# Performance work log

Measured on AMD Instinct MI355X. Metric: run time of the kernel, lower is better.

## Reference

```python
import jax, jax.numpy as jnp
import numpy as np

B, T, C, H = 4, 2048, 1024, 16
HD = C // H  # head_size = 64
EPS = 1e-5


def setup_inputs() -> dict:
    key = jax.random.key(0)
    ks = jax.random.split(key, 16)
    s_c = 1.0 / np.sqrt(C)
    s_4c = 1.0 / np.sqrt(4 * C)
    return {
        "x": jax.random.normal(ks[0], (B, T, C), jnp.float32),
        # per-head projections, stored [H, C, HD] (already in x@W orientation)
        "wq": jax.random.uniform(ks[1], (H, C, HD), jnp.float32, -s_c, s_c),
        "wk": jax.random.uniform(ks[2], (H, C, HD), jnp.float32, -s_c, s_c),
        "wv": jax.random.uniform(ks[3], (H, C, HD), jnp.float32, -s_c, s_c),
        "w_proj": jax.random.uniform(ks[4], (C, C), jnp.float32, -s_c, s_c),
        "b_proj": jax.random.uniform(ks[5], (C,), jnp.float32, -s_c, s_c),
        "w1": jax.random.uniform(ks[6], (C, 4 * C), jnp.float32, -s_c, s_c),
        "b1": jax.random.uniform(ks[7], (4 * C,), jnp.float32, -s_c, s_c),
        "w2": jax.random.uniform(ks[8], (4 * C, C), jnp.float32, -s_4c, s_4c),
        "b2": jax.random.uniform(ks[9], (C,), jnp.float32, -s_4c, s_4c),
        "ln1_g": jnp.ones((C,), jnp.float32),
        "ln1_b": jnp.zeros((C,), jnp.float32),
        "ln2_g": jnp.ones((C,), jnp.float32),
        "ln2_b": jnp.zeros((C,), jnp.float32),
    }


def layer_norm(x, g, b):
    mu = jnp.mean(x, axis=-1, keepdims=True)
    var = jnp.mean(jnp.square(x - mu), axis=-1, keepdims=True)
    return (x - mu) * jax.lax.rsqrt(var + EPS) * g + b


def reference(x, wq, wk, wv, w_proj, b_proj, w1, b1, w2, b2, ln1_g, ln1_b, ln2_g, ln2_b):
    Bc, Tc, Cc = x.shape
    h = layer_norm(x, ln1_g, ln1_b)
    q = jnp.einsum("btc,hcd->bhtd", h, wq)
    k = jnp.einsum("btc,hcd->bhtd", h, wk)
    v = jnp.einsum("btc,hcd->bhtd", h, wv)
    scale = HD ** -0.5
    wei = jnp.einsum("bhtd,bhsd->bhts", q, k) * scale  # [B,H,T,T]
    causal = jnp.tril(jnp.ones((Tc, Tc), bool))
    wei = jnp.where(causal, wei, -jnp.inf)
    wei = jax.nn.softmax(wei, axis=-1)
    att = jnp.einsum("bhts,bhsd->bhtd", wei, v)
    att = att.transpose(0, 2, 1, 3).reshape(Bc, Tc, Cc)  # concat heads
    x = x + att @ w_proj + b_proj
    h2 = layer_norm(x, ln2_g, ln2_b)
    ff = jax.nn.relu(h2 @ w1 + b1) @ w2 + b2
    return x + ff
```

## Files before the change

kernel.cpp:

```cpp
#include <hip/hip_runtime.h>


#define B_ 4
#define T_ 2048
#define C_ 1024
#define H_ 16
#define BT_ 8192

typedef __attribute__((ext_vector_type(8))) __bf16 bf16x8;
typedef __attribute__((ext_vector_type(4))) __bf16 bf16x4;
typedef __attribute__((ext_vector_type(4))) float f32x4;

#define WAIT_LGKM0 asm volatile("s_waitcnt lgkmcnt(0)" ::: "memory")
#define WAIT_VM(N) asm volatile("s_waitcnt vmcnt(" #N ")" ::: "memory")
#define NOSTG ((void)0)

__device__ __forceinline__ void gload_lds16(const void* g, void* l) {
  __builtin_amdgcn_global_load_lds((const __attribute__((address_space(1))) void*)g,
                                   (__attribute__((address_space(3))) void*)l, 16, 0, 0);
}

__device__ __forceinline__ void block_sync() {
  asm volatile("" ::: "memory");
  __builtin_amdgcn_s_barrier();
  asm volatile("" ::: "memory");
}

__global__ __launch_bounds__(256) void transpose_f32_bf16(
    const float* __restrict__ in, __bf16* __restrict__ out,
    int R, int Cc, long inBatch, long outBatch) {
  __shared__ float tile[32][33];
  const int tx = threadIdx.x, ty = threadIdx.y;
  in += (long)blockIdx.z * inBatch;
  out += (long)blockIdx.z * outBatch;
  const int r0 = blockIdx.y * 32, c0 = blockIdx.x * 32;
#pragma unroll
  for (int i = 0; i < 4; i++)
    tile[ty + i * 8][tx] = in[(long)(r0 + ty + i * 8) * Cc + c0 + tx];
  __syncthreads();
#pragma unroll
  for (int i = 0; i < 4; i++)
    out[(long)(c0 + ty + i * 8) * R + r0 + tx] = (__bf16)tile[tx][ty + i * 8];
}

__global__ __launch_bounds__(256) void ln_fwd(const float* __restrict__ x,
                                              const float* __restrict__ g,
                                              const float* __restrict__ bta,
                                              __bf16* __restrict__ out) {
  const long row = blockIdx.x;
  const int tid = threadIdx.x;
  float4 v = ((const float4*)(x + row * C_))[tid];
  float vals[4] = {v.x, v.y, v.z, v.w};
  float s = vals[0] + vals[1] + vals[2] + vals[3];
  float s2 = vals[0] * vals[0] + vals[1] * vals[1] + vals[2] * vals[2] + vals[3] * vals[3];
#pragma unroll
  for (int o = 1; o < 64; o <<= 1) {
    s += __shfl_xor(s, o);
    s2 += __shfl_xor(s2, o);
  }
  __shared__ float red[8];
  const int lane = tid & 63, wid = tid >> 6;
  if (lane == 0) { red[wid] = s; red[wid + 4] = s2; }
  __syncthreads();
  const float S = red[0] + red[1] + red[2] + red[3];
  const float S2 = red[4] + red[5] + red[6] + red[7];
  const float mu = S * (1.0f / C_);
  const float var = S2 * (1.0f / C_) - mu * mu;
  const float rs = rsqrtf(var + 1e-5f);
  bf16x4 o4;
#pragma unroll
  for (int j = 0; j < 4; j++) {
    const int c = tid * 4 + j;
    o4[j] = (__bf16)((vals[j] - mu) * rs * g[c] + bta[c]);
  }
  *(bf16x4*)(out + row * C_ + tid * 4) = o4;
}

template <int EPI, int SPLITK>
__global__ __launch_bounds__(512, 2) void gemm2x(
    const __bf16* __restrict__ A, const __bf16* __restrict__ Bt,
    void* out0, void* out1, void* out2,
    const float* __restrict__ bias, const float* __restrict__ resid,
    int M, int N, int K, int nwg) {
  __shared__ __bf16 sm[65536];
  __bf16* ldsA = &sm[0];
  __bf16* ldsB = &sm[32768];
  const int tid = threadIdx.x, lane = tid & 63, wid = tid >> 6;
  const int wm = wid >> 2, wn = wid & 3;
  const int l15 = lane & 15, qtr = lane >> 4;
  const int q8 = nwg >> 3;
  int wg = (blockIdx.x & 7) * q8 + (blockIdx.x >> 3);
  int k0 = 0, KS = K;
  if (SPLITK) { KS = K >> 1; k0 = (wg >> 7) * KS; wg &= 127; }
  const int mBlocks = M >> 8;
  const long mBase = (long)(wg % mBlocks) * 256;
  const long nBase = (long)(wg / mBlocks) * 256;
  const int NT = KS >> 6;

  f32x4 acc[8][4] = {};
  bf16x8 bfr[4];

  const int posRd = (qtr ^ ((l15 >> 1) & 3)) * 8;
  const int aRdB = (wm * 128 + l15) * 32 + posRd;
  const int bRdB = (wn * 64 + l15) * 32 + posRd;

  const int spos = (tid & 3) ^ ((tid >> 3) & 3);
  const __bf16* aS0 = A + (mBase + (tid >> 2)) * (long)K + k0 + spos * 8;
  const __bf16* aS1 = aS0 + 128 * (long)K;
  const __bf16* bS0 = Bt + (nBase + (tid >> 2)) * (long)K + k0 + spos * 8;
  const __bf16* bS1 = bS0 + 128 * (long)K;

#define STGA(BUF, KH, KT)                                                                     \
  do {                                                                                        \
    gload_lds16(aS0 + (KT) * 64 + (KH) * 32, ldsA + ((BUF) * 2 + (KH)) * 8192 + tid * 8);     \
    gload_lds16(aS1 + (KT) * 64 + (KH) * 32, ldsA + ((BUF) * 2 + (KH)) * 8192 + 4096 + tid * 8); \
  } while (0)
#define STGB(BUF, KH, KT)                                                                     \
  do {                                                                                        \
    gload_lds16(bS0 + (KT) * 64 + (KH) * 32, ldsB + ((BUF) * 2 + (KH)) * 8192 + tid * 8);     \
    gload_lds16(bS1 + (KT) * 64 + (KH) * 32, ldsB + ((BUF) * 2 + (KH)) * 8192 + 4096 + tid * 8); \
  } while (0)

#define PH(BUF, KH, RFH, WAITOP, STG)                                                        \
  do {                                                                                       \
    const __bf16* sA_ = ldsA + ((BUF) * 2 + (KH)) * 8192;                                    \
    const __bf16* sB_ = ldsB + ((BUF) * 2 + (KH)) * 8192;                                    \
    bf16x8 af0 = *(const bf16x8*)&sA_[aRdB + (RFH) * 2048];                                  \
    bf16x8 af1 = *(const bf16x8*)&sA_[aRdB + (RFH) * 2048 + 512];                            \
    bf16x8 af2 = *(const bf16x8*)&sA_[aRdB + (RFH) * 2048 + 1024];                           \
    bf16x8 af3 = *(const bf16x8*)&sA_[aRdB + (RFH) * 2048 + 1536];                           \
    if ((RFH) == 0) {                                                                        \
      bfr[0] = *(const bf16x8*)&sB_[bRdB];                                                   \
      bfr[1] = *(const bf16x8*)&sB_[bRdB + 512];                                             \
      bfr[2] = *(const bf16x8*)&sB_[bRdB + 1024];                                            \
      bfr[3] = *(const bf16x8*)&sB_[bRdB + 1536];                                            \
    }                                                                                        \
    STG;                                                                                     \
    WAITOP;                                                                                  \
    block_sync();                                                                            \
    WAIT_LGKM0;                                                                              \
    __builtin_amdgcn_sched_barrier(0);                                                       \
    __builtin_amdgcn_s_setprio(1);                                                           \
    acc[(RFH)*4+0][0] = __builtin_amdgcn_mfma_f32_16x16x32_bf16(af0, bfr[0], acc[(RFH)*4+0][0], 0, 0, 0); \
    acc[(RFH)*4+0][1] = __builtin_amdgcn_mfma_f32_16x16x32_bf16(af0, bfr[1], acc[(RFH)*4+0][1], 0, 0, 0); \
    acc[(RFH)*4+0][2] = __builtin_amdgcn_mfma_f32_16x16x32_bf16(af0, bfr[2], acc[(RFH)*4+0][2], 0, 0, 0); \
    acc[(RFH)*4+0][3] = __builtin_amdgcn_mfma_f32_16x16x32_bf16(af0, bfr[3], acc[(RFH)*4+0][3], 0, 0, 0); \
    acc[(RFH)*4+1][0] = __builtin_amdgcn_mfma_f32_16x16x32_bf16(af1, bfr[0], acc[(RFH)*4+1][0], 0, 0, 0); \
    acc[(RFH)*4+1][1] = __builtin_amdgcn_mfma_f32_16x16x32_bf16(af1, bfr[1], acc[(RFH)*4+1][1], 0, 0, 0); \
    acc[(RFH)*4+1][2] = __builtin_amdgcn_mfma_f32_16x16x32_bf16(af1, bfr[2], acc[(RFH)*4+1][2], 0, 0, 0); \
    acc[(RFH)*4+1][3] = __builtin_amdgcn_mfma_f32_16x16x32_bf16(af1, bfr[3], acc[(RFH)*4+1][3], 0, 0, 0); \
    acc[(RFH)*4+2][0] = __builtin_amdgcn_mfma_f32_16x16x32_bf16(af2, bfr[0], acc[(RFH)*4+2][0], 0, 0, 0); \
    acc[(RFH)*4+2][1] = __builtin_amdgcn_mfma_f32_16x16x32_bf16(af2, bfr[1], acc[(RFH)*4+2][1], 0, 0, 0); \
    acc[(RFH)*4+2][2] = __builtin_amdgcn_mfma_f32_16x16x32_bf16(af2, bfr[2], acc[(RFH)*4+2][2], 0, 0, 0); \
    acc[(RFH)*4+2][3] = __builtin_amdgcn_mfma_f32_16x16x32_bf16(af2, bfr[3], acc[(RFH)*4+2][3], 0, 0, 0); \
    acc[(RFH)*4+3][0] = __builtin_amdgcn_mfma_f32_16x16x32_bf16(af3, bfr[0], acc[(RFH)*4+3][0], 0, 0, 0); \
    acc[(RFH)*4+3][1] = __builtin_amdgcn_mfma_f32_16x16x32_bf16(af3, bfr[1], acc[(RFH)*4+3][1], 0, 0, 0); \
    acc[(RFH)*4+3][2] = __builtin_amdgcn_mfma_f32_16x16x32_bf16(af3, bfr[2], acc[(RFH)*4+3][2], 0, 0, 0); \
    acc[(RFH)*4+3][3] = __builtin_amdgcn_mfma_f32_16x16x32_bf16(af3, bfr[3], acc[(RFH)*4+3][3], 0, 0, 0); \
    __builtin_amdgcn_s_setprio(0);                                                           \
    block_sync();                                                                            \
  } while (0)

  STGA(0, 0, 0); STGB(0, 0, 0);
  STGA(0, 1, 0); STGB(0, 1, 0);
  STGA(1, 0, 1); STGB(1, 0, 1);
  WAIT_VM(8);
  block_sync();

  int b = 0;
  for (int t = 0; t + 2 < NT; ++t) {
    PH(b, 0, 0, NOSTG, STGA(b ^ 1, 1, t + 1));
    PH(b, 0, 1, WAIT_VM(8), STGB(b ^ 1, 1, t + 1));
    PH(b, 1, 0, NOSTG, STGA(b, 0, t + 2));
    PH(b, 1, 1, WAIT_VM(8), STGB(b, 0, t + 2));
    b ^= 1;
  }
  PH(0, 0, 0, NOSTG, STGA(1, 1, NT - 1));
  PH(0, 0, 1, WAIT_VM(8), STGB(1, 1, NT - 1));
  PH(0, 1, 0, NOSTG, NOSTG);
  PH(0, 1, 1, WAIT_VM(4), NOSTG);
  PH(1, 0, 0, NOSTG, NOSTG);
  PH(1, 0, 1, WAIT_VM(0), NOSTG);
  PH(1, 1, 0, NOSTG, NOSTG);
  PH(1, 1, 1, WAIT_VM(0), NOSTG);

#undef PH
#undef STGA
#undef STGB

  if (EPI == 0) {
    __bf16* outB = (__bf16*)out0;
#pragma unroll
    for (int cf = 0; cf < 4; cf++) {
      const long gc = nBase + wn * 64 + cf * 16 + l15;
      const float bv = bias[gc];
#pragma unroll
      for (int rf = 0; rf < 8; rf++) {
        const long gr0 = mBase + wm * 128 + rf * 16 + qtr * 4;
#pragma unroll
        for (int r = 0; r < 4; r++)
          outB[(gr0 + r) * (long)N + gc] = (__bf16)fmaxf(acc[rf][cf][r] + bv, 0.0f);
      }
    }
  } else if (EPI == 2) {
    float* outF = (float*)out0;
#pragma unroll
    for (int cf = 0; cf < 4; cf++) {
      const long gc = nBase + wn * 64 + cf * 16 + l15;
      const float bv = bias[gc];
#pragma unroll
      for (int rf = 0; rf < 8; rf++) {
        const long gr0 = mBase + wm * 128 + rf * 16 + qtr * 4;
#pragma unroll
        for (int r = 0; r < 4; r++)
          outF[(gr0 + r) * (long)N + gc] = acc[rf][cf][r] + bv + resid[(gr0 + r) * (long)N + gc];
      }
    }
  } else if (EPI == 3) {
    float* outF = (float*)out0;
#pragma unroll
    for (int cf = 0; cf < 4; cf++) {
      const long gc = nBase + wn * 64 + cf * 16 + l15;
      const float bv = (k0 == 0) ? bias[gc] : 0.0f;
#pragma unroll
      for (int rf = 0; rf < 8; rf++) {
        const long gr0 = mBase + wm * 128 + rf * 16 + qtr * 4;
#pragma unroll
        for (int r = 0; r < 4; r++)
          atomicAdd(&outF[(gr0 + r) * (long)N + gc], acc[rf][cf][r] + bv);
      }
    }
  } else {
    const int seg = (int)(nBase >> 10);
#pragma unroll
    for (int cf = 0; cf < 4; cf++) {
      const long gc = nBase + wn * 64 + cf * 16 + l15;
      const long cc = gc & 1023;
#pragma unroll
      for (int rf = 0; rf < 8; rf++) {
        const long gr0 = mBase + wm * 128 + rf * 16 + qtr * 4;
        if (seg == 0) {
          __bf16* Qb = (__bf16*)out0;
#pragma unroll
          for (int r = 0; r < 4; r++) Qb[(gr0 + r) * 1024 + cc] = (__bf16)acc[rf][cf][r];
        } else if (seg == 1) {
          __bf16* Kb = (__bf16*)out1;
#pragma unroll
          for (int r = 0; r < 4; r++) Kb[(gr0 + r) * 1024 + cc] = (__bf16)acc[rf][cf][r];
        } else {
          __bf16* Vtg = (__bf16*)out2;
          bf16x4 v4;
#pragma unroll
          for (int r = 0; r < 4; r++) v4[r] = (__bf16)acc[rf][cf][r];
          *(bf16x4*)&Vtg[cc * (long)BT_ + gr0] = v4;
        }
      }
    }
  }
}

#define PSTR 72
__global__ __launch_bounds__(512, 6) void attn_fwd2(
    const __bf16* __restrict__ Qg, const __bf16* __restrict__ Kg,
    const __bf16* __restrict__ Vtg, __bf16* __restrict__ O) {
  __shared__ __bf16 Ks[2][64 * 64];
  __shared__ __bf16 Vs[2][64 * 64];
  __shared__ __bf16 Ps[128 * PSTR];
  const int tid = threadIdx.x, lane = tid & 63, wid = tid >> 6;
  const int bh = blockIdx.x, b = bh >> 4, h = bh & 15;
  const int qx = 15 - blockIdx.y;
  const int qBase = qx * 128;
  const int qw = qBase + wid * 16;
  const int qwTop = qw + 15;
  const long bT = (long)b * T_;
  const int l15 = lane & 15, qtr = lane >> 4;
  const int q_lane = qw + l15;

  const int srow = tid >> 3;
  const int schunk = (tid & 7) ^ (srow & 7);
  const __bf16* kSrcBase = Kg + (bT + srow) * C_ + h * 64 + schunk * 8;
  const __bf16* vSrcBase = Vtg + (long)(h * 64 + srow) * BT_ + bT + schunk * 8;
  __bf16* kDst = &Ks[0][tid * 8];
  __bf16* vDst = &Vs[0][tid * 8];
  const int bufStride = 64 * 64;

  bf16x8 q0s, q1s;
  {
    const float SC = 0.125f * 1.44269504089f;
    bf16x8 r0 = *(const bf16x8*)(Qg + (bT + q_lane) * C_ + h * 64 + qtr * 8);
    bf16x8 r1 = *(const bf16x8*)(Qg + (bT + q_lane) * C_ + h * 64 + 32 + qtr * 8);
#pragma unroll
    for (int j = 0; j < 8; j++) {
      q0s[j] = (__bf16)((float)r0[j] * SC);
      q1s[j] = (__bf16)((float)r1[j] * SC);
    }
  }

  f32x4 o[4] = {};
  float m_ = -1e30f, l_ = 0.0f;
  const int nkt = 2 * qx + 2;

  gload_lds16(kSrcBase, kDst);
  gload_lds16(vSrcBase, vDst);
  __syncthreads();

  int buf = 0;
  for (int t = 0; t < nkt; t++) {
    const int k0 = t * 64;
    if (t + 1 < nkt) {
      const long koff = (long)(k0 + 64);
      gload_lds16(kSrcBase + koff * C_, kDst + (buf ^ 1) * bufStride);
      gload_lds16(vSrcBase + koff, vDst + (buf ^ 1) * bufStride);
    }
    if (k0 <= qwTop) {
      const __bf16* ks = Ks[buf];
      const __bf16* vs = Vs[buf];
      f32x4 sT[4] = {};
      __builtin_amdgcn_s_setprio(1);
#pragma unroll
      for (int kb = 0; kb < 4; kb++) {
        bf16x8 aK0 = *(const bf16x8*)&ks[(kb * 16 + l15) * 64 + ((qtr ^ (l15 & 7)) * 8)];
        bf16x8 aK1 = *(const bf16x8*)&ks[(kb * 16 + l15) * 64 + (((4 + qtr) ^ (l15 & 7)) * 8)];
        sT[kb] = __builtin_amdgcn_mfma_f32_16x16x32_bf16(aK0, q0s, sT[kb], 0, 0, 0);
        sT[kb] = __builtin_amdgcn_mfma_f32_16x16x32_bf16(aK1, q1s, sT[kb], 0, 0, 0);
      }
      __builtin_amdgcn_s_setprio(0);
      if (k0 + 63 > qw) {
#pragma unroll
        for (int kb = 0; kb < 4; kb++)
#pragma unroll
          for (int r = 0; r < 4; r++)
            if (k0 + kb * 16 + qtr * 4 + r > q_lane) sT[kb][r] = -1e30f;
      }
      float mx = -1e30f;
#pragma unroll
      for (int kb = 0; kb < 4; kb++)
#pragma unroll
        for (int r = 0; r < 4; r++) mx = fmaxf(mx, sT[kb][r]);
      mx = fmaxf(mx, __shfl_xor(mx, 16));
      mx = fmaxf(mx, __shfl_xor(mx, 32));
      const bool defer = __all(mx - m_ <= 8.0f);
      const float mnew = defer ? m_ : fmaxf(m_, mx);
      float psum = 0.0f;
#pragma unroll
      for (int kb = 0; kb < 4; kb++)
#pragma unroll
        for (int r = 0; r < 4; r++) {
          const float pv = exp2f(sT[kb][r] - mnew);
          psum += pv;
          Ps[(wid * 16 + l15) * PSTR + kb * 16 + qtr * 4 + r] = (__bf16)pv;
        }
      psum += __shfl_xor(psum, 16);
      psum += __shfl_xor(psum, 32);
      if (defer) {
        l_ += psum;
      } else {
        const float fac = exp2f(m_ - mnew);
        l_ = l_ * fac + psum;
        m_ = mnew;
#pragma unroll
        for (int r = 0; r < 4; r++) {
          const float fr = __shfl(fac, (lane & 48) + qtr * 4 + r);
#pragma unroll
          for (int dg = 0; dg < 4; dg++) o[dg][r] *= fr;
        }
      }
      __builtin_amdgcn_s_setprio(1);
#pragma unroll
      for (int s = 0; s < 2; s++) {
        bf16x8 aP = *(const bf16x8*)&Ps[(wid * 16 + l15) * PSTR + s * 32 + qtr * 8];
#pragma unroll
        for (int dg = 0; dg < 4; dg++) {
          bf16x8 bV = *(const bf16x8*)&vs[(dg * 16 + l15) * 64 + (((s * 4 + qtr) ^ (l15 & 7)) * 8)];
          o[dg] = __builtin_amdgcn_mfma_f32_16x16x32_bf16(aP, bV, o[dg], 0, 0, 0);
        }
      }
      __builtin_amdgcn_s_setprio(0);
    }
    __syncthreads();
    buf ^= 1;
  }

  const float linv = 1.0f / l_;
#pragma unroll
  for (int r = 0; r < 4; r++) {
    const float lr = __shfl(linv, (lane & 48) + qtr * 4 + r);
    const long row = bT + qw + qtr * 4 + r;
#pragma unroll
    for (int dg = 0; dg < 4; dg++)
      O[row * C_ + h * 64 + dg * 16 + l15] = (__bf16)(o[dg][r] * lr);
  }
}

extern "C" void kernel_launch(void* const* d_in, const int* in_sizes, int n_in,
                              void* d_out, int out_size, void* d_ws, size_t ws_size,
                              hipStream_t stream) {
  const float* x = (const float*)d_in[0];
  const float* wq = (const float*)d_in[1];
  const float* wk = (const float*)d_in[2];
  const float* wv = (const float*)d_in[3];
  const float* wproj = (const float*)d_in[4];
  const float* bproj = (const float*)d_in[5];
  const float* w1 = (const float*)d_in[6];
  const float* b1 = (const float*)d_in[7];
  const float* w2 = (const float*)d_in[8];
  const float* b2 = (const float*)d_in[9];
  const float* g1 = (const float*)d_in[10];
  const float* be1 = (const float*)d_in[11];
  const float* g2 = (const float*)d_in[12];
  const float* be2 = (const float*)d_in[13];

  char* ws = (char*)d_ws;
  const size_t MB = 1024ull * 1024ull;
  __bf16* h1 = (__bf16*)(ws + 0);
  __bf16* Qb = (__bf16*)(ws + 16 * MB);
  __bf16* Kb = (__bf16*)(ws + 32 * MB);
  __bf16* Vtg = (__bf16*)(ws + 48 * MB);
  __bf16* ff1 = (__bf16*)(ws + 32 * MB);
  __bf16* wqt = (__bf16*)(ws + 96 * MB);
  __bf16* wkt = (__bf16*)(ws + 98 * MB);
  __bf16* wvt = (__bf16*)(ws + 100 * MB);
  __bf16* wpt = (__bf16*)(ws + 102 * MB);
  __bf16* w1t = (__bf16*)(ws + 104 * MB);
  __bf16* w2t = (__bf16*)(ws + 112 * MB);
  __bf16* att = h1;
  __bf16* h2 = Qb;
  float* xout = (float*)d_out;

  dim3 tb(32, 8);
  transpose_f32_bf16<<<dim3(2, 32, 16), tb, 0, stream>>>(wq, wqt, 1024, 64, 1024 * 64, 64 * 1024);
  transpose_f32_bf16<<<dim3(2, 32, 16), tb, 0, stream>>>(wk, wkt, 1024, 64, 1024 * 64, 64 * 1024);
  transpose_f32_bf16<<<dim3(2, 32, 16), tb, 0, stream>>>(wv, wvt, 1024, 64, 1024 * 64, 64 * 1024);
  transpose_f32_bf16<<<dim3(32, 32, 1), tb, 0, stream>>>(wproj, wpt, 1024, 1024, 0, 0);
  transpose_f32_bf16<<<dim3(128, 32, 1), tb, 0, stream>>>(w1, w1t, 1024, 4096, 0, 0);
  transpose_f32_bf16<<<dim3(32, 128, 1), tb, 0, stream>>>(w2, w2t, 4096, 1024, 0, 0);

  ln_fwd<<<8192, 256, 0, stream>>>(x, g1, be1, h1);
  gemm2x<1, 0><<<384, 512, 0, stream>>>(h1, wqt, Qb, Kb, Vtg, nullptr, nullptr, 8192, 3072, 1024, 384);
  attn_fwd2<<<dim3(64, 16), 512, 0, stream>>>(Qb, Kb, Vtg, att);
  gemm2x<2, 0><<<128, 512, 0, stream>>>(att, wpt, xout, nullptr, nullptr, bproj, x, 8192, 1024, 1024, 128);
  ln_fwd<<<8192, 256, 0, stream>>>(xout, g2, be2, h2);
  gemm2x<0, 0><<<512, 512, 0, stream>>>(h2, w1t, ff1, nullptr, nullptr, b1, nullptr, 8192, 4096, 1024, 512);
  gemm2x<3, 1><<<256, 512, 0, stream>>>(ff1, w2t, xout, nullptr, nullptr, b2, nullptr, 8192, 1024, 4096, 256);
}
```

Before: 436.6 us.

## Restructure GEMM LDS layout to 64-wide K tiles with new pipeline schedule

Rewrites the bf16 GEMM main loop. LDS staging now uses 64-element K rows with an 8-chunk XOR swizzle in place of two 32-wide halves, and A/B fragments are read as pairs of k-chunks feeding two MFMAs each. The pipeline is regrouped into four sub-phases per tile with separate A and B prefetch slots, aiming to reduce LDS bank conflicts and barrier overhead. Separately, the attention kernel now writes P as packed bf16x4 stores with precomputed pointers instead of scalar stores. The new schedule and wait counts risk hazards or extra register pressure from holding eight A and eight B fragments.

```diff
diff --git a/kernel.cpp b/kernel.cpp
--- a/kernel.cpp
+++ b/kernel.cpp
@@ -13,7 +13,6 @@
 
 #define WAIT_LGKM0 asm volatile("s_waitcnt lgkmcnt(0)" ::: "memory")
 #define WAIT_VM(N) asm volatile("s_waitcnt vmcnt(" #N ")" ::: "memory")
-#define NOSTG ((void)0)
 
 __device__ __forceinline__ void gload_lds16(const void* g, void* l) {
   __builtin_amdgcn_global_load_lds((const __attribute__((address_space(1))) void*)g,
@@ -77,7 +76,7 @@
 }
 
 template <int EPI, int SPLITK>
-__global__ __launch_bounds__(512, 2) void gemm2x(
+__global__ __launch_bounds__(512, 2) void gemm256(
     const __bf16* __restrict__ A, const __bf16* __restrict__ Bt,
     void* out0, void* out1, void* out2,
     const float* __restrict__ bias, const float* __restrict__ resid,
@@ -87,7 +86,7 @@
   __bf16* ldsB = &sm[32768];
   const int tid = threadIdx.x, lane = tid & 63, wid = tid >> 6;
   const int wm = wid >> 2, wn = wid & 3;
-  const int l15 = lane & 15, qtr = lane >> 4;
+  const int l15 = lane & 15, qtr = lane >> 4, l7 = l15 & 7;
   const int q8 = nwg >> 3;
   int wg = (blockIdx.x & 7) * q8 + (blockIdx.x >> 3);
   int k0 = 0, KS = K;
@@ -96,97 +95,117 @@
   const long mBase = (long)(wg % mBlocks) * 256;
   const long nBase = (long)(wg / mBlocks) * 256;
   const int NT = KS >> 6;
+  const long Kl = K;
 
   f32x4 acc[8][4] = {};
-  bf16x8 bfr[4];
-
-  const int posRd = (qtr ^ ((l15 >> 1) & 3)) * 8;
-  const int aRdB = (wm * 128 + l15) * 32 + posRd;
-  const int bRdB = (wn * 64 + l15) * 32 + posRd;
-
-  const int spos = (tid & 3) ^ ((tid >> 3) & 3);
-  const __bf16* aS0 = A + (mBase + (tid >> 2)) * (long)K + k0 + spos * 8;
-  const __bf16* aS1 = aS0 + 128 * (long)K;
-  const __bf16* bS0 = Bt + (nBase + (tid >> 2)) * (long)K + k0 + spos * 8;
-  const __bf16* bS1 = bS0 + 128 * (long)K;
-
-#define STGA(BUF, KH, KT)                                                                     \
-  do {                                                                                        \
-    gload_lds16(aS0 + (KT) * 64 + (KH) * 32, ldsA + ((BUF) * 2 + (KH)) * 8192 + tid * 8);     \
-    gload_lds16(aS1 + (KT) * 64 + (KH) * 32, ldsA + ((BUF) * 2 + (KH)) * 8192 + 4096 + tid * 8); \
-  } while (0)
-#define STGB(BUF, KH, KT)                                                                     \
-  do {                                                                                        \
-    gload_lds16(bS0 + (KT) * 64 + (KH) * 32, ldsB + ((BUF) * 2 + (KH)) * 8192 + tid * 8);     \
-    gload_lds16(bS1 + (KT) * 64 + (KH) * 32, ldsB + ((BUF) * 2 + (KH)) * 8192 + 4096 + tid * 8); \
-  } while (0)
-
-#define PH(BUF, KH, RFH, WAITOP, STG)                                                        \
+  bf16x8 a8[8], b8[8];
+
+  const int pk0 = (qtr ^ l7) * 8;
+  const int pk1 = ((4 + qtr) ^ l7) * 8;
+  const int aoff = l15 * 64;
+  const int bH = wn >> 1, bQ = (wn & 1) * 4096;
+
+  const int srow = tid >> 3;
+  const int schunk = (tid & 7) ^ (srow & 7);
+  const __bf16* aSrc = A + (mBase + srow) * Kl + k0 + schunk * 8;
+  const __bf16* bSrc = Bt + (nBase + srow) * Kl + k0 + schunk * 8;
+
+#define STG_A(BUF, H, T2)                                                                    \
   do {                                                                                       \
-    const __bf16* sA_ = ldsA + ((BUF) * 2 + (KH)) * 8192;                                    \
-    const __bf16* sB_ = ldsB + ((BUF) * 2 + (KH)) * 8192;                                    \
-    bf16x8 af0 = *(const bf16x8*)&sA_[aRdB + (RFH) * 2048];                                  \
-    bf16x8 af1 = *(const bf16x8*)&sA_[aRdB + (RFH) * 2048 + 512];                            \
-    bf16x8 af2 = *(const bf16x8*)&sA_[aRdB + (RFH) * 2048 + 1024];                           \
-    bf16x8 af3 = *(const bf16x8*)&sA_[aRdB + (RFH) * 2048 + 1536];                           \
-    if ((RFH) == 0) {                                                                        \
-      bfr[0] = *(const bf16x8*)&sB_[bRdB];                                                   \
-      bfr[1] = *(const bf16x8*)&sB_[bRdB + 512];                                             \
-      bfr[2] = *(const bf16x8*)&sB_[bRdB + 1024];                                            \
-      bfr[3] = *(const bf16x8*)&sB_[bRdB + 1536];                                            \
-    }                                                                                        \
-    STG;                                                                                     \
-    WAITOP;                                                                                  \
-    block_sync();                                                                            \
-    WAIT_LGKM0;                                                                              \
-    __builtin_amdgcn_sched_barrier(0);                                                       \
-    __builtin_amdgcn_s_setprio(1);                                                           \
-    acc[(RFH)*4+0][0] = __builtin_amdgcn_mfma_f32_16x16x32_bf16(af0, bfr[0], acc[(RFH)*4+0][0], 0, 0, 0); \
-    acc[(RFH)*4+0][1] = __builtin_amdgcn_mfma_f32_16x16x32_bf16(af0, bfr[1], acc[(RFH)*4+0][1], 0, 0, 0); \
-    acc[(RFH)*4+0][2] = __builtin_amdgcn_mfma_f32_16x16x32_bf16(af0, bfr[2], acc[(RFH)*4+0][2], 0, 0, 0); \
-    acc[(RFH)*4+0][3] = __builtin_amdgcn_mfma_f32_16x16x32_bf16(af0, bfr[3], acc[(RFH)*4+0][3], 0, 0, 0); \
-    acc[(RFH)*4+1][0] = __builtin_amdgcn_mfma_f32_16x16x32_bf16(af1, bfr[0], acc[(RFH)*4+1][0], 0, 0, 0); \
-    acc[(RFH)*4+1][1] = __builtin_amdgcn_mfma_f32_16x16x32_bf16(af1, bfr[1], acc[(RFH)*4+1][1], 0, 0, 0); \
-    acc[(RFH)*4+1][2] = __builtin_amdgcn_mfma_f32_16x16x32_bf16(af1, bfr[2], acc[(RFH)*4+1][2], 0, 0, 0); \
-    acc[(RFH)*4+1][3] = __builtin_amdgcn_mfma_f32_16x16x32_bf16(af1, bfr[3], acc[(RFH)*4+1][3], 0, 0, 0); \
-    acc[(RFH)*4+2][0] = __builtin_amdgcn_mfma_f32_16x16x32_bf16(af2, bfr[0], acc[(RFH)*4+2][0], 0, 0, 0); \
-    acc[(RFH)*4+2][1] = __builtin_amdgcn_mfma_f32_16x16x32_bf16(af2, bfr[1], acc[(RFH)*4+2][1], 0, 0, 0); \
-    acc[(RFH)*4+2][2] = __builtin_amdgcn_mfma_f32_16x16x32_bf16(af2, bfr[2], acc[(RFH)*4+2][2], 0, 0, 0); \
-    acc[(RFH)*4+2][3] = __builtin_amdgcn_mfma_f32_16x16x32_bf16(af2, bfr[3], acc[(RFH)*4+2][3], 0, 0, 0); \
-    acc[(RFH)*4+3][0] = __builtin_amdgcn_mfma_f32_16x16x32_bf16(af3, bfr[0], acc[(RFH)*4+3][0], 0, 0, 0); \
-    acc[(RFH)*4+3][1] = __builtin_amdgcn_mfma_f32_16x16x32_bf16(af3, bfr[1], acc[(RFH)*4+3][1], 0, 0, 0); \
-    acc[(RFH)*4+3][2] = __builtin_amdgcn_mfma_f32_16x16x32_bf16(af3, bfr[2], acc[(RFH)*4+3][2], 0, 0, 0); \
-    acc[(RFH)*4+3][3] = __builtin_amdgcn_mfma_f32_16x16x32_bf16(af3, bfr[3], acc[(RFH)*4+3][3], 0, 0, 0); \
-    __builtin_amdgcn_s_setprio(0);                                                           \
-    block_sync();                                                                            \
-  } while (0)
-
-  STGA(0, 0, 0); STGB(0, 0, 0);
-  STGA(0, 1, 0); STGB(0, 1, 0);
-  STGA(1, 0, 1); STGB(1, 0, 1);
-  WAIT_VM(8);
+    gload_lds16(aSrc + (long)((H) * 128) * Kl + (long)(T2) * 64,                             \
+                ldsA + ((BUF) * 2 + (H)) * 8192 + tid * 8);                                  \
+    gload_lds16(aSrc + (long)((H) * 128 + 64) * Kl + (long)(T2) * 64,                        \
+                ldsA + ((BUF) * 2 + (H)) * 8192 + 4096 + tid * 8);                           \
+  } while (0)
+#define STG_B(BUF, H, T2)                                                                    \
+  do {                                                                                       \
+    gload_lds16(bSrc + (long)((H) * 128) * Kl + (long)(T2) * 64,                             \
+                ldsB + ((BUF) * 2 + (H)) * 8192 + tid * 8);                                  \
+    gload_lds16(bSrc + (long)((H) * 128 + 64) * Kl + (long)(T2) * 64,                        \
+                ldsB + ((BUF) * 2 + (H)) * 8192 + 4096 + tid * 8);                           \
+  } while (0)
+
+#define RD_A(BUF, GRP)                                                                       \
+  do {                                                                                       \
+    const __bf16* pA_ = &ldsA[((BUF) * 2 + wm) * 8192 + aoff];                               \
+    a8[0] = *(const bf16x8*)&pA_[((GRP) * 4 + 0) * 1024 + pk0];                              \
+    a8[1] = *(const bf16x8*)&pA_[((GRP) * 4 + 0) * 1024 + pk1];                              \
+    a8[2] = *(const bf16x8*)&pA_[((GRP) * 4 + 1) * 1024 + pk0];                              \
+    a8[3] = *(const bf16x8*)&pA_[((GRP) * 4 + 1) * 1024 + pk1];                              \
+    a8[4] = *(const bf16x8*)&pA_[((GRP) * 4 + 2) * 1024 + pk0];                              \
+    a8[5] = *(const bf16x8*)&pA_[((GRP) * 4 + 2) * 1024 + pk1];                              \
+    a8[6] = *(const bf16x8*)&pA_[((GRP) * 4 + 3) * 1024 + pk0];                              \
+    a8[7] = *(const bf16x8*)&pA_[((GRP) * 4 + 3) * 1024 + pk1];                              \
+  } while (0)
+#define RD_B(BUF, GRP)                                                                       \
+  do {                                                                                       \
+    const __bf16* pB_ = &ldsB[((BUF) * 2 + bH) * 8192 + bQ + aoff];                          \
+    b8[(GRP) * 4 + 0] = *(const bf16x8*)&pB_[((GRP) * 2 + 0) * 1024 + pk0];                  \
+    b8[(GRP) * 4 + 1] = *(const bf16x8*)&pB_[((GRP) * 2 + 0) * 1024 + pk1];                  \
+    b8[(GRP) * 4 + 2] = *(const bf16x8*)&pB_[((GRP) * 2 + 1) * 1024 + pk0];                  \
+    b8[(GRP) * 4 + 3] = *(const bf16x8*)&pB_[((GRP) * 2 + 1) * 1024 + pk1];                  \
+  } while (0)
+
+#define MFQ(RFG, CFG)                                                                                          \
+  do {                                                                                                         \
+    acc[(RFG)*4+0][(CFG)*2+0] = __builtin_amdgcn_mfma_f32_16x16x32_bf16(a8[0], b8[(CFG)*4+0], acc[(RFG)*4+0][(CFG)*2+0], 0, 0, 0); \
+    acc[(RFG)*4+0][(CFG)*2+0] = __builtin_amdgcn_mfma_f32_16x16x32_bf16(a8[1], b8[(CFG)*4+1], acc[(RFG)*4+0][(CFG)*2+0], 0, 0, 0); \
+    acc[(RFG)*4+0][(CFG)*2+1] = __builtin_amdgcn_mfma_f32_16x16x32_bf16(a8[0], b8[(CFG)*4+2], acc[(RFG)*4+0][(CFG)*2+1], 0, 0, 0); \
+    acc[(RFG)*4+0][(CFG)*2+1] = __builtin_amdgcn_mfma_f32_16x16x32_bf16(a8[1], b8[(CFG)*4+3], acc[(RFG)*4+0][(CFG)*2+1], 0, 0, 0); \
+    acc[(RFG)*4+1][(CFG)*2+0] = __builtin_amdgcn_mfma_f32_16x16x32_bf16(a8[2], b8[(CFG)*4+0], acc[(RFG)*4+1][(CFG)*2+0], 0, 0, 0); \
+    acc[(RFG)*4+1][(CFG)*2+0] = __builtin_amdgcn_mfma_f32_16x16x32_bf16(a8[3], b8[(CFG)*4+1], acc[(RFG)*4+1][(CFG)*2+0], 0, 0, 0); \
+    acc[(RFG)*4+1][(CFG)*2+1] = __builtin_amdgcn_mfma_f32_16x16x32_bf16(a8[2], b8[(CFG)*4+2], acc[(RFG)*4+1][(CFG)*2+1], 0, 0, 0); \
+    acc[(RFG)*4+1][(CFG)*2+1] = __builtin_amdgcn_mfma_f32_16x16x32_bf16(a8[3], b8[(CFG)*4+3], acc[(RFG)*4+1][(CFG)*2+1], 0, 0, 0); \
+    acc[(RFG)*4+2][(CFG)*2+0] = __builtin_amdgcn_mfma_f32_16x16x32_bf16(a8[4], b8[(CFG)*4+0], acc[(RFG)*4+2][(CFG)*2+0], 0, 0, 0); \
+    acc[(RFG)*4+2][(CFG)*2+0] = __builtin_amdgcn_mfma_f32_16x16x32_bf16(a8[5], b8[(CFG)*4+1], acc[(RFG)*4+2][(CFG)*2+0], 0, 0, 0); \
+    acc[(RFG)*4+2][(CFG)*2+1] = __builtin_amdgcn_mfma_f32_16x16x32_bf16(a8[4], b8[(CFG)*4+2], acc[(RFG)*4+2][(CFG)*2+1], 0, 0, 0); \
+    acc[(RFG)*4+2][(CFG)*2+1] = __builtin_amdgcn_mfma_f32_16x16x32_bf16(a8[5], b8[(CFG)*4+3], acc[(RFG)*4+2][(CFG)*2+1], 0, 0, 0); \
+    acc[(RFG)*4+3][(CFG)*2+0] = __builtin_amdgcn_mfma_f32_16x16x32_bf16(a8[6], b8[(CFG)*4+0], acc[(RFG)*4+3][(CFG)*2+0], 0, 0, 0); \
+    acc[(RFG)*4+3][(CFG)*2+0] = __builtin_amdgcn_mfma_f32_16x16x32_bf16(a8[7], b8[(CFG)*4+1], acc[(RFG)*4+3][(CFG)*2+0], 0, 0, 0); \
+    acc[(RFG)*4+3][(CFG)*2+1] = __builtin_amdgcn_mfma_f32_16x16x32_bf16(a8[6], b8[(CFG)*4+2], acc[(RFG)*4+3][(CFG)*2+1], 0, 0, 0); \
+    acc[(RFG)*4+3][(CFG)*2+1] = __builtin_amdgcn_mfma_f32_16x16x32_bf16(a8[7], b8[(CFG)*4+3], acc[(RFG)*4+3][(CFG)*2+1], 0, 0, 0); \
+  } while (0)
+
+#define SP1 __builtin_amdgcn_s_setprio(1)
+#define SP0 __builtin_amdgcn_s_setprio(0)
+#define SCHED0 __builtin_amdgcn_sched_barrier(0)
+
+#define TILE(BUF, T)                                                                         \
+  do {                                                                                       \
+                                                                      \
+    RD_A(BUF, 0); RD_B(BUF, 0);                                                              \
+    if ((T) + 1 < NT) STG_A((BUF) ^ 1, 0, (T) + 1);                                          \
+    block_sync(); WAIT_LGKM0; SCHED0; SP1; MFQ(0, 0); SP0; block_sync();                     \
+                                                                      \
+    RD_B(BUF, 1);                                                                            \
+    if ((T) + 1 < NT) STG_A((BUF) ^ 1, 1, (T) + 1);                                          \
+    block_sync(); WAIT_LGKM0; SCHED0; SP1; MFQ(0, 1); SP0; block_sync();                     \
+                                                                      \
+    RD_A(BUF, 1);                                                                            \
+    if ((T) + 2 < NT) STG_B(BUF, 0, (T) + 2);                                                \
+    block_sync(); WAIT_LGKM0; SCHED0; SP1; MFQ(1, 0); SP0; block_sync();                     \
+                                                                      \
+    if ((T) + 2 < NT) { STG_B(BUF, 1, (T) + 2); WAIT_VM(4); } else { WAIT_VM(0); }           \
+    block_sync(); SCHED0; SP1; MFQ(1, 1); SP0; block_sync();                                 \
+  } while (0)
+
+  STG_A(0, 0, 0); STG_A(0, 1, 0);
+  STG_B(0, 0, 0); STG_B(0, 1, 0);
+  STG_B(1, 0, 1); STG_B(1, 1, 1);
+  WAIT_VM(4);
   block_sync();
 
-  int b = 0;
-  for (int t = 0; t + 2 < NT; ++t) {
-    PH(b, 0, 0, NOSTG, STGA(b ^ 1, 1, t + 1));
-    PH(b, 0, 1, WAIT_VM(8), STGB(b ^ 1, 1, t + 1));
-    PH(b, 1, 0, NOSTG, STGA(b, 0, t + 2));
-    PH(b, 1, 1, WAIT_VM(8), STGB(b, 0, t + 2));
-    b ^= 1;
-  }
-  PH(0, 0, 0, NOSTG, STGA(1, 1, NT - 1));
-  PH(0, 0, 1, WAIT_VM(8), STGB(1, 1, NT - 1));
-  PH(0, 1, 0, NOSTG, NOSTG);
-  PH(0, 1, 1, WAIT_VM(4), NOSTG);
-  PH(1, 0, 0, NOSTG, NOSTG);
-  PH(1, 0, 1, WAIT_VM(0), NOSTG);
-  PH(1, 1, 0, NOSTG, NOSTG);
-  PH(1, 1, 1, WAIT_VM(0), NOSTG);
-
-#undef PH
-#undef STGA
-#undef STGB
+  for (int t = 0; t < NT; t += 2) {
+    TILE(0, t);
+    TILE(1, t + 1);
+  }
+
+#undef TILE
+#undef MFQ
+#undef RD_A
+#undef RD_B
+#undef STG_A
+#undef STG_B
 
   if (EPI == 0) {
     __bf16* outB = (__bf16*)out0;
@@ -284,6 +303,9 @@
   __bf16* vDst = &Vs[0][tid * 8];
   const int bufStride = 64 * 64;
 
+  __bf16* psW = &Ps[(wid * 16 + l15) * PSTR + qtr * 4];
+  const __bf16* psR = &Ps[(wid * 16 + l15) * PSTR + qtr * 8];
+
   bf16x8 q0s, q1s;
   {
     const float SC = 0.125f * 1.44269504089f;
@@ -343,13 +365,16 @@
       const float mnew = defer ? m_ : fmaxf(m_, mx);
       float psum = 0.0f;
 #pragma unroll
-      for (int kb = 0; kb < 4; kb++)
+      for (int kb = 0; kb < 4; kb++) {
+        bf16x4 p4;
 #pragma unroll
         for (int r = 0; r < 4; r++) {
           const float pv = exp2f(sT[kb][r] - mnew);
           psum += pv;
-          Ps[(wid * 16 + l15) * PSTR + kb * 16 + qtr * 4 + r] = (__bf16)pv;
+          p4[r] = (__bf16)pv;
         }
+        *(bf16x4*)&psW[kb * 16] = p4;
+      }
       psum += __shfl_xor(psum, 16);
       psum += __shfl_xor(psum, 32);
       if (defer) {
@@ -368,7 +393,7 @@
       __builtin_amdgcn_s_setprio(1);
 #pragma unroll
       for (int s = 0; s < 2; s++) {
-        bf16x8 aP = *(const bf16x8*)&Ps[(wid * 16 + l15) * PSTR + s * 32 + qtr * 8];
+        bf16x8 aP = *(const bf16x8*)&psR[s * 32];
 #pragma unroll
         for (int dg = 0; dg < 4; dg++) {
           bf16x8 bV = *(const bf16x8*)&vs[(dg * 16 + l15) * 64 + (((s * 4 + qtr) ^ (l15 & 7)) * 8)];
@@ -436,10 +461,10 @@
   transpose_f32_bf16<<<dim3(32, 128, 1), tb, 0, stream>>>(w2, w2t, 4096, 1024, 0, 0);
 
   ln_fwd<<<8192, 256, 0, stream>>>(x, g1, be1, h1);
-  gemm2x<1, 0><<<384, 512, 0, stream>>>(h1, wqt, Qb, Kb, Vtg, nullptr, nullptr, 8192, 3072, 1024, 384);
+  gemm256<1, 0><<<384, 512, 0, stream>>>(h1, wqt, Qb, Kb, Vtg, nullptr, nullptr, 8192, 3072, 1024, 384);
   attn_fwd2<<<dim3(64, 16), 512, 0, stream>>>(Qb, Kb, Vtg, att);
-  gemm2x<2, 0><<<128, 512, 0, stream>>>(att, wpt, xout, nullptr, nullptr, bproj, x, 8192, 1024, 1024, 128);
+  gemm256<2, 0><<<128, 512, 0, stream>>>(att, wpt, xout, nullptr, nullptr, bproj, x, 8192, 1024, 1024, 128);
   ln_fwd<<<8192, 256, 0, stream>>>(xout, g2, be2, h2);
-  gemm2x<0, 0><<<512, 512, 0, stream>>>(h2, w1t, ff1, nullptr, nullptr, b1, nullptr, 8192, 4096, 1024, 512);
-  gemm2x<3, 1><<<256, 512, 0, stream>>>(ff1, w2t, xout, nullptr, nullptr, b2, nullptr, 8192, 1024, 4096, 256);
-}
+  gemm256<0, 0><<<512, 512, 0, stream>>>(h2, w1t, ff1, nullptr, nullptr, b1, nullptr, 8192, 4096, 1024, 512);
+  gemm256<3, 1><<<256, 512, 0, stream>>>(ff1, w2t, xout, nullptr, nullptr, b2, nullptr, 8192, 1024, 4096, 256);
+}
```

Measured after the change: 430.2 us. About the same (-1.5%).
